# Optimization experiments

Measured on AMD Instinct MI355X. Metric: run time of the kernel, lower is better.

Reference implementation:

```python
import jax, jax.numpy as jnp
import numpy as np

H = 50  # hidden_dim
L = 4   # num_layers

def setup_inputs() -> dict:
    key = jax.random.key(0)
    ks = jax.random.split(key, 12)
    B, T, D = 2048, 512, 1
    s0 = 1.0 / np.sqrt(H)  # PyTorch GRU init scale
    x = jax.random.normal(ks[0], (B, T, D), dtype=jnp.float32)
    # layer 0 (input size 1)
    W_ih0 = jax.random.uniform(ks[1], (3 * H, D), minval=-s0, maxval=s0, dtype=jnp.float32)
    W_hh0 = jax.random.uniform(ks[2], (3 * H, H), minval=-s0, maxval=s0, dtype=jnp.float32)
    b_ih0 = jax.random.uniform(ks[3], (3 * H,), minval=-s0, maxval=s0, dtype=jnp.float32)
    b_hh0 = jax.random.uniform(ks[4], (3 * H,), minval=-s0, maxval=s0, dtype=jnp.float32)
    # layers 1..3 stacked (input size H)
    W_ih = jax.random.uniform(ks[5], (L - 1, 3 * H, H), minval=-s0, maxval=s0, dtype=jnp.float32)
    W_hh = jax.random.uniform(ks[6], (L - 1, 3 * H, H), minval=-s0, maxval=s0, dtype=jnp.float32)
    b_ih = jax.random.uniform(ks[7], (L - 1, 3 * H), minval=-s0, maxval=s0, dtype=jnp.float32)
    b_hh = jax.random.uniform(ks[8], (L - 1, 3 * H), minval=-s0, maxval=s0, dtype=jnp.float32)
    fc_w = jax.random.uniform(ks[9], (1, H), minval=-s0, maxval=s0, dtype=jnp.float32)
    fc_b = jax.random.uniform(ks[10], (1,), minval=-s0, maxval=s0, dtype=jnp.float32)
    return {"x": x, "W_ih0": W_ih0, "W_hh0": W_hh0, "b_ih0": b_ih0, "b_hh0": b_hh0,
            "W_ih": W_ih, "W_hh": W_hh, "b_ih": b_ih, "b_hh": b_hh,
            "fc_w": fc_w, "fc_b": fc_b}


def _gru_layer(x_seq, Wih, Whh, bih, bhh):
    # x_seq: [B, T, Din] -> outputs [B, T, H]. PyTorch GRU cell math.
    gx = jnp.einsum('btd,gd->btg', x_seq, Wih) + bih  # [B, T, 3H], precomputed input gates
    gx = jnp.transpose(gx, (1, 0, 2))  # [T, B, 3H]
    h0 = jnp.zeros((x_seq.shape[0], H), dtype=x_seq.dtype)

    def step(h, gxt):
        gh = h @ Whh.T + bhh  # [B, 3H]
        xr, xz, xn = jnp.split(gxt, 3, axis=-1)
        hr, hz, hn = jnp.split(gh, 3, axis=-1)
        r = jax.nn.sigmoid(xr + hr)
        z = jax.nn.sigmoid(xz + hz)
        n = jnp.tanh(xn + r * hn)
        h_new = (1.0 - z) * n + z * h
        return h_new, h_new

    _, hs = jax.lax.scan(step, h0, gx)  # hs: [T, B, H]
    return jnp.transpose(hs, (1, 0, 2))  # [B, T, H]


def reference(x, W_ih0, W_hh0, b_ih0, b_hh0, W_ih, W_hh, b_ih, b_hh, fc_w, fc_b):
    out = _gru_layer(x, W_ih0, W_hh0, b_ih0, b_hh0)
    for l in range(L - 1):  # eval mode: dropout inactive
        out = _gru_layer(out, W_ih[l], W_hh[l], b_ih[l], b_hh[l])
    last = out[:, -1, :]  # [B, H]
    logits = last @ fc_w.T + fc_b  # [B, 1]
    return jax.nn.sigmoid(logits)
```

## Files before the change

kernel.cpp:

```cpp
#include <hip/hip_runtime.h>
#include <hip/hip_fp16.h>

#define HDIM  50
#define G3    150
#define TSEQ  512
#define BATCH 2048
#define NB    8
#define NLAY  4
#define NT    12

typedef _Float16 f16x8 __attribute__((ext_vector_type(8)));
typedef float    f32x4 __attribute__((ext_vector_type(4)));

#define MFMA(a,b,c) __builtin_amdgcn_mfma_f32_16x16x32_f16((a),(b),(c),0,0,0)

static __device__ inline unsigned pk2(float a, float b) {
    return __builtin_bit_cast(unsigned, __builtin_amdgcn_cvt_pkrtz(a, b));
}
static __device__ inline float rcpf(float x) { return __builtin_amdgcn_rcpf(x); }

#if __has_builtin(__builtin_amdgcn_exp2f)
static __device__ inline float ex2(float x) { return __builtin_amdgcn_exp2f(x); }
#else
static __device__ inline float ex2(float x) {
    float r; asm volatile("v_exp_f32 %0, %1" : "=v"(r) : "v"(x)); return r;
}
#endif
static __device__ inline float dpp8(float x) {
    return __builtin_bit_cast(float, __builtin_amdgcn_mov_dpp(
        __builtin_bit_cast(int, x), 0x128, 0xf, 0xf, true));
}

#define SCL_RZ (-1.44269504f)
#define SCL_N  ( 2.88539008f)

__global__ __launch_bounds__(256, 1)
void gru_fused1w(const float* __restrict__ xin,
                 const float* __restrict__ Wih0, const float* __restrict__ Whh0,
                 const float* __restrict__ bih0, const float* __restrict__ bhh0,
                 const float* __restrict__ WihL, const float* __restrict__ WhhL,
                 const float* __restrict__ bihL, const float* __restrict__ bhhL,
                 const float* __restrict__ fcw,  const float* __restrict__ fcb,
                 float* __restrict__ out)
{
    const int tid  = threadIdx.x;
    const int lay  = tid >> 6;
    const int lane = tid & 63;
    const int lb   = lane & 15;
    const int lg   = lane >> 4;
    const int b0   = blockIdx.x * NB;
    const int lbc  = (lb < NB) ? lb : (NB - 1);
    const bool lo  = (lb < 8);

    __shared__ __align__(16) _Float16 h_lds[NLAY][2][16][72];
    __shared__ float x_row[NB][516];

    const float* Wih = (lay==0) ? Wih0 : WihL + (size_t)(lay-1)*G3*HDIM;
    const float* Whh = (lay==0) ? Whh0 : WhhL + (size_t)(lay-1)*G3*HDIM;
    const float* bih = (lay==0) ? bih0 : bihL + (lay-1)*G3;
    const float* bhh = (lay==0) ? bhh0 : bhhL + (lay-1)*G3;

    f16x8 a_hh[NT][2], a_ih[NT][2];
#pragma unroll
    for (int mt = 0; mt < NT; ++mt) {
        const int  ur = (mt & 3)*16 + lb;
        const bool rv = ur < HDIM;
        const int  gr = 50*(mt >> 2) + (rv ? ur : 0);
        const float scl = (mt < 8) ? SCL_RZ : SCL_N;
#pragma unroll
        for (int kt = 0; kt < 2; ++kt) {
            f16x8 fh, fi;
#pragma unroll
            for (int j = 0; j < 8; ++j) {
                const int k = 32*kt + 8*lg + j;
                float vh = 0.f, vi = 0.f;
                if (rv) {
                    if (k < HDIM)       vh = Whh[gr*HDIM + k];
                    else if (k == HDIM) vh = bhh[gr];
                    if (lay == 0) {
                        if (kt == 0 && k == 0)      vi = Wih[gr];
                        else if (kt == 0 && k == 1) vi = bih[gr];
                    } else {
                        if (k < HDIM)       vi = Wih[gr*HDIM + k];
                        else if (k == HDIM) vi = bih[gr];
                    }
                }
                fh[j] = (_Float16)(vh * scl); fi[j] = (_Float16)(vi * scl);
            }
            a_hh[mt][kt] = fh; a_ih[mt][kt] = fi;
        }
    }

    for (int k = tid; k < NB*TSEQ; k += 256)
        x_row[k >> 9][k & 511] = xin[(size_t)(b0 + (k >> 9))*TSEQ + (k & 511)];
    for (int k = tid; k < NLAY*2*16*72; k += 256)
        ((_Float16*)h_lds)[k] = (_Float16)(((k % 72) == HDIM) ? 1.f : 0.f);

    float hold[4][4];
#pragma unroll
    for (int m = 0; m < 4; ++m)
#pragma unroll
        for (int i = 0; i < 4; ++i) hold[m][i] = 0.f;
    __syncthreads();

    f16x8 bh0 = *(const f16x8*)&h_lds[lay][1][lb][8*lg];
    f16x8 bh1 = *(const f16x8*)&h_lds[lay][1][lb][32 + 8*lg];
    f16x8 bx0{}, bx1{};
    if (lay == 0) {
#pragma unroll
        for (int j = 0; j < 8; ++j) bx0[j] = (_Float16)0.f;
        if (lg == 0) { bx0[0] = (_Float16)x_row[lbc][0]; bx0[1] = (_Float16)1.f; }
    } else {
        bx0 = *(const f16x8*)&h_lds[lay-1][1][lb][8*lg];
        bx1 = *(const f16x8*)&h_lds[lay-1][1][lb][32 + 8*lg];
    }
    const f32x4 Z4 = {0.f, 0.f, 0.f, 0.f};

    for (int s = 0; s < TSEQ + NLAY - 1; ++s) {
        const int t = s - lay;
        if (t >= 0 && t < TSEQ) {
            f32x4 acc[NT], accx[4];
#pragma unroll
            for (int mt = 0; mt < NT; ++mt) acc[mt] = MFMA(a_hh[mt][0], bh0, Z4);
#pragma unroll
            for (int mt = 0; mt < NT; ++mt) acc[mt] = MFMA(a_hh[mt][1], bh1, acc[mt]);
#pragma unroll
            for (int mt = 0; mt < 8; ++mt)  acc[mt] = MFMA(a_ih[mt][0], bx0, acc[mt]);
#pragma unroll
            for (int m = 0; m < 4; ++m)     accx[m] = MFMA(a_ih[8+m][0], bx0, Z4);
            if (lay != 0) {
#pragma unroll
                for (int mt = 0; mt < 8; ++mt) acc[mt] = MFMA(a_ih[mt][1], bx1, acc[mt]);
#pragma unroll
                for (int m = 0; m < 4; ++m)    accx[m] = MFMA(a_ih[8+m][1], bx1, accx[m]);
            }

#pragma unroll
            for (int mt = 0; mt < 8; ++mt) {
#pragma unroll
                for (int ip = 0; ip < 2; ++ip) {
                    if (((mt & 3) == 3) && ip == 1) continue;
                    const float v0 = acc[mt][2*ip], v1 = acc[mt][2*ip+1];
                    const float w  = dpp8(v1);
                    const float sg = rcpf(1.f + ex2(lo ? v0 : w));
                    const float sb = dpp8(sg);
                    acc[mt][2*ip]   = lo ? sg : sb;
                    acc[mt][2*ip+1] = lo ? sb : sg;
                }
            }

            float hp[4][4];
#pragma unroll
            for (int m = 0; m < 4; ++m) {
#pragma unroll
                for (int ip = 0; ip < 2; ++ip) {
                    if (m == 3 && ip == 1) { hp[3][2] = 0.f; hp[3][3] = 0.f; continue; }
                    const int i0 = 2*ip, i1 = 2*ip + 1;
                    const float vp0 = accx[m][i0] + acc[m][i0] * acc[8+m][i0];
                    const float vp1 = accx[m][i1] + acc[m][i1] * acc[8+m][i1];
                    const float w   = dpp8(vp1);
                    const float n_  = 1.f - 2.f*rcpf(ex2(lo ? vp0 : w) + 1.f);
                    const float nb  = dpp8(n_);
                    const float n0  = lo ? n_ : nb;
                    const float n1  = lo ? nb : n_;
                    hp[m][i0] = fmaf(acc[4+m][i0], hold[m][i0] - n0, n0);
                    hp[m][i1] = fmaf(acc[4+m][i1], hold[m][i1] - n1, n1);
                    hold[m][i0] = hp[m][i0];
                    hold[m][i1] = hp[m][i1];
                }
            }

            {
                _Float16* hrow = &h_lds[lay][s & 1][lb][0];
#pragma unroll
                for (int m = 0; m < 3; ++m) {
                    uint2 q; q.x = pk2(hp[m][0], hp[m][1]);
                             q.y = pk2(hp[m][2], hp[m][3]);
                    *(uint2*)&hrow[16*m + 4*lg] = q;
                }
                if (lg == 0)
                    *(unsigned*)&hrow[48] = pk2(hp[3][0], hp[3][1]);
            }
        }
        __syncthreads();

        const int pb = s & 1;
        bh0 = *(const f16x8*)&h_lds[lay][pb][lb][8*lg];
        bh1 = *(const f16x8*)&h_lds[lay][pb][lb][32 + 8*lg];
        if (lay == 0) {
            const int tt = (s+1 < TSEQ) ? s+1 : TSEQ-1;
            if (lg == 0) bx0[0] = (_Float16)x_row[lbc][tt];
        } else {
            bx0 = *(const f16x8*)&h_lds[lay-1][pb][lb][8*lg];
            bx1 = *(const f16x8*)&h_lds[lay-1][pb][lb][32 + 8*lg];
        }
    }

    if (tid < NB) {
        float sacc = fcb[0];
#pragma unroll
        for (int j = 0; j < HDIM; ++j)
            sacc = fmaf((float)h_lds[NLAY-1][0][tid][j], fcw[j], sacc);
        out[b0 + tid] = rcpf(1.f + __expf(-sacc));
    }
}

extern "C" void kernel_launch(void* const* d_in, const int* in_sizes, int n_in,
                              void* d_out, int out_size, void* d_ws, size_t ws_size,
                              hipStream_t stream) {
    const float* x     = (const float*)d_in[0];
    const float* W_ih0 = (const float*)d_in[1];
    const float* W_hh0 = (const float*)d_in[2];
    const float* b_ih0 = (const float*)d_in[3];
    const float* b_hh0 = (const float*)d_in[4];
    const float* W_ih  = (const float*)d_in[5];
    const float* W_hh  = (const float*)d_in[6];
    const float* b_ih  = (const float*)d_in[7];
    const float* b_hh  = (const float*)d_in[8];
    const float* fc_w  = (const float*)d_in[9];
    const float* fc_b  = (const float*)d_in[10];
    float* out = (float*)d_out;

    dim3 grid(BATCH / NB), block(256);
    gru_fused1w<<<grid, block, 0, stream>>>(
        x, W_ih0, W_hh0, b_ih0, b_hh0,
        W_ih, W_hh, b_ih, b_hh, fc_w, fc_b, out);
}
```

Before: 596.1 us.

## Process two timesteps per barrier with 4-slot hidden-state ring buffer

```diff
diff --git a/kernel.cpp b/kernel.cpp
--- a/kernel.cpp
+++ b/kernel.cpp
@@ -52,7 +52,7 @@
     const int lbc  = (lb < NB) ? lb : (NB - 1);
     const bool lo  = (lb < 8);
 
-    __shared__ __align__(16) _Float16 h_lds[NLAY][2][16][72];
+    __shared__ __align__(16) _Float16 hsl[NLAY][4][16][72];
     __shared__ float x_row[NB][516];
 
     const float* Wih = (lay==0) ? Wih0 : WihL + (size_t)(lay-1)*G3*HDIM;
@@ -93,8 +93,8 @@
 
     for (int k = tid; k < NB*TSEQ; k += 256)
         x_row[k >> 9][k & 511] = xin[(size_t)(b0 + (k >> 9))*TSEQ + (k & 511)];
-    for (int k = tid; k < NLAY*2*16*72; k += 256)
-        ((_Float16*)h_lds)[k] = (_Float16)(((k % 72) == HDIM) ? 1.f : 0.f);
+    for (int k = tid; k < NLAY*4*16*72; k += 256)
+        ((_Float16*)hsl)[k] = (_Float16)(((k % 72) == HDIM) ? 1.f : 0.f);
 
     float hold[4][4];
 #pragma unroll
@@ -103,104 +103,106 @@
         for (int i = 0; i < 4; ++i) hold[m][i] = 0.f;
     __syncthreads();
 
-    f16x8 bh0 = *(const f16x8*)&h_lds[lay][1][lb][8*lg];
-    f16x8 bh1 = *(const f16x8*)&h_lds[lay][1][lb][32 + 8*lg];
-    f16x8 bx0{}, bx1{};
-    if (lay == 0) {
-#pragma unroll
-        for (int j = 0; j < 8; ++j) bx0[j] = (_Float16)0.f;
-        if (lg == 0) { bx0[0] = (_Float16)x_row[lbc][0]; bx0[1] = (_Float16)1.f; }
-    } else {
-        bx0 = *(const f16x8*)&h_lds[lay-1][1][lb][8*lg];
-        bx1 = *(const f16x8*)&h_lds[lay-1][1][lb][32 + 8*lg];
-    }
+    f16x8 bh0 = *(const f16x8*)&hsl[lay][3][lb][8*lg];
+    f16x8 bh1 = *(const f16x8*)&hsl[lay][3][lb][32 + 8*lg];
     const f32x4 Z4 = {0.f, 0.f, 0.f, 0.f};
 
-    for (int s = 0; s < TSEQ + NLAY - 1; ++s) {
-        const int t = s - lay;
-        if (t >= 0 && t < TSEQ) {
-            f32x4 acc[NT], accx[4];
-#pragma unroll
-            for (int mt = 0; mt < NT; ++mt) acc[mt] = MFMA(a_hh[mt][0], bh0, Z4);
-#pragma unroll
-            for (int mt = 0; mt < NT; ++mt) acc[mt] = MFMA(a_hh[mt][1], bh1, acc[mt]);
-#pragma unroll
-            for (int mt = 0; mt < 8; ++mt)  acc[mt] = MFMA(a_ih[mt][0], bx0, acc[mt]);
-#pragma unroll
-            for (int m = 0; m < 4; ++m)     accx[m] = MFMA(a_ih[8+m][0], bx0, Z4);
-            if (lay != 0) {
-#pragma unroll
-                for (int mt = 0; mt < 8; ++mt) acc[mt] = MFMA(a_ih[mt][1], bx1, acc[mt]);
-#pragma unroll
-                for (int m = 0; m < 4; ++m)    accx[m] = MFMA(a_ih[8+m][1], bx1, accx[m]);
-            }
-
-#pragma unroll
-            for (int mt = 0; mt < 8; ++mt) {
-#pragma unroll
-                for (int ip = 0; ip < 2; ++ip) {
-                    if (((mt & 3) == 3) && ip == 1) continue;
-                    const float v0 = acc[mt][2*ip], v1 = acc[mt][2*ip+1];
-                    const float w  = dpp8(v1);
-                    const float sg = rcpf(1.f + ex2(lo ? v0 : w));
-                    const float sb = dpp8(sg);
-                    acc[mt][2*ip]   = lo ? sg : sb;
-                    acc[mt][2*ip+1] = lo ? sb : sg;
+    auto STEP = [&](int t, f16x8 bxk0, f16x8 bxk1) {
+        f32x4 acc[NT], accx[4];
+#pragma unroll
+        for (int mt = 0; mt < NT; ++mt) acc[mt] = MFMA(a_hh[mt][0], bh0, Z4);
+#pragma unroll
+        for (int mt = 0; mt < NT; ++mt) acc[mt] = MFMA(a_hh[mt][1], bh1, acc[mt]);
+#pragma unroll
+        for (int mt = 0; mt < 8; ++mt)  acc[mt] = MFMA(a_ih[mt][0], bxk0, acc[mt]);
+#pragma unroll
+        for (int m = 0; m < 4; ++m)     accx[m] = MFMA(a_ih[8+m][0], bxk0, Z4);
+        if (lay != 0) {
+#pragma unroll
+            for (int mt = 0; mt < 8; ++mt) acc[mt] = MFMA(a_ih[mt][1], bxk1, acc[mt]);
+#pragma unroll
+            for (int m = 0; m < 4; ++m)    accx[m] = MFMA(a_ih[8+m][1], bxk1, accx[m]);
+        }
+
+#pragma unroll
+        for (int mt = 0; mt < 8; ++mt) {
+#pragma unroll
+            for (int ip = 0; ip < 2; ++ip) {
+                if (((mt & 3) == 3) && ip == 1) continue;
+                const float v0 = acc[mt][2*ip], v1 = acc[mt][2*ip+1];
+                const float w  = dpp8(v1);
+                const float sg = rcpf(1.f + ex2(lo ? v0 : w));
+                const float sb = dpp8(sg);
+                acc[mt][2*ip]   = lo ? sg : sb;
+                acc[mt][2*ip+1] = lo ? sb : sg;
+            }
+        }
+
+        float hp[4][4];
+#pragma unroll
+        for (int m = 0; m < 4; ++m) {
+#pragma unroll
+            for (int ip = 0; ip < 2; ++ip) {
+                if (m == 3 && ip == 1) { hp[3][2] = 0.f; hp[3][3] = 0.f; continue; }
+                const int i0 = 2*ip, i1 = 2*ip + 1;
+                const float vp0 = accx[m][i0] + acc[m][i0] * acc[8+m][i0];
+                const float vp1 = accx[m][i1] + acc[m][i1] * acc[8+m][i1];
+                const float w   = dpp8(vp1);
+                const float n_  = 1.f - 2.f*rcpf(ex2(lo ? vp0 : w) + 1.f);
+                const float nb  = dpp8(n_);
+                const float n0  = lo ? n_ : nb;
+                const float n1  = lo ? nb : n_;
+                hp[m][i0] = fmaf(acc[4+m][i0], hold[m][i0] - n0, n0);
+                hp[m][i1] = fmaf(acc[4+m][i1], hold[m][i1] - n1, n1);
+                hold[m][i0] = hp[m][i0];
+                hold[m][i1] = hp[m][i1];
+            }
+        }
+
+        {
+            _Float16* hrow = &hsl[lay][t & 3][lb][0];
+#pragma unroll
+            for (int m = 0; m < 3; ++m) {
+                uint2 q; q.x = pk2(hp[m][0], hp[m][1]);
+                         q.y = pk2(hp[m][2], hp[m][3]);
+                *(uint2*)&hrow[16*m + 4*lg] = q;
+            }
+            if (lg == 0)
+                *(unsigned*)&hrow[48] = pk2(hp[3][0], hp[3][1]);
+        }
+        bh0 = *(const f16x8*)&hsl[lay][t & 3][lb][8*lg];
+        bh1 = *(const f16x8*)&hsl[lay][t & 3][lb][32 + 8*lg];
+    };
+
+    for (int s = 0; s < TSEQ/2 + NLAY - 1; ++s) {
+        if (s >= lay && s < lay + TSEQ/2) {
+            const int t0 = 2*(s - lay);
+            f16x8 bxa0{}, bxa1{}, bxb0{}, bxb1{};
+            if (lay == 0) {
+#pragma unroll
+                for (int j = 0; j < 8; ++j) { bxa0[j] = (_Float16)0.f; bxb0[j] = (_Float16)0.f; }
+                if (lg == 0) {
+                    bxa0[0] = (_Float16)x_row[lbc][t0];     bxa0[1] = (_Float16)1.f;
+                    bxb0[0] = (_Float16)x_row[lbc][t0 + 1]; bxb0[1] = (_Float16)1.f;
                 }
-            }
-
-            float hp[4][4];
-#pragma unroll
-            for (int m = 0; m < 4; ++m) {
-#pragma unroll
-                for (int ip = 0; ip < 2; ++ip) {
-                    if (m == 3 && ip == 1) { hp[3][2] = 0.f; hp[3][3] = 0.f; continue; }
-                    const int i0 = 2*ip, i1 = 2*ip + 1;
-                    const float vp0 = accx[m][i0] + acc[m][i0] * acc[8+m][i0];
-                    const float vp1 = accx[m][i1] + acc[m][i1] * acc[8+m][i1];
-                    const float w   = dpp8(vp1);
-                    const float n_  = 1.f - 2.f*rcpf(ex2(lo ? vp0 : w) + 1.f);
-                    const float nb  = dpp8(n_);
-                    const float n0  = lo ? n_ : nb;
-                    const float n1  = lo ? nb : n_;
-                    hp[m][i0] = fmaf(acc[4+m][i0], hold[m][i0] - n0, n0);
-                    hp[m][i1] = fmaf(acc[4+m][i1], hold[m][i1] - n1, n1);
-                    hold[m][i0] = hp[m][i0];
-                    hold[m][i1] = hp[m][i1];
-                }
-            }
-
-            {
-                _Float16* hrow = &h_lds[lay][s & 1][lb][0];
-#pragma unroll
-                for (int m = 0; m < 3; ++m) {
-                    uint2 q; q.x = pk2(hp[m][0], hp[m][1]);
-                             q.y = pk2(hp[m][2], hp[m][3]);
-                    *(uint2*)&hrow[16*m + 4*lg] = q;
-                }
-                if (lg == 0)
-                    *(unsigned*)&hrow[48] = pk2(hp[3][0], hp[3][1]);
-            }
+            } else {
+                const int sa = t0 & 3, sb = (t0 + 1) & 3;
+                bxa0 = *(const f16x8*)&hsl[lay-1][sa][lb][8*lg];
+                bxa1 = *(const f16x8*)&hsl[lay-1][sa][lb][32 + 8*lg];
+                bxb0 = *(const f16x8*)&hsl[lay-1][sb][lb][8*lg];
+                bxb1 = *(const f16x8*)&hsl[lay-1][sb][lb][32 + 8*lg];
+            }
+            STEP(t0,     bxa0, bxa1);
+            STEP(t0 + 1, bxb0, bxb1);
         }
         __syncthreads();
-
-        const int pb = s & 1;
-        bh0 = *(const f16x8*)&h_lds[lay][pb][lb][8*lg];
-        bh1 = *(const f16x8*)&h_lds[lay][pb][lb][32 + 8*lg];
-        if (lay == 0) {
-            const int tt = (s+1 < TSEQ) ? s+1 : TSEQ-1;
-            if (lg == 0) bx0[0] = (_Float16)x_row[lbc][tt];
-        } else {
-            bx0 = *(const f16x8*)&h_lds[lay-1][pb][lb][8*lg];
-            bx1 = *(const f16x8*)&h_lds[lay-1][pb][lb][32 + 8*lg];
-        }
     }
 
     if (tid < NB) {
         float sacc = fcb[0];
 #pragma unroll
         for (int j = 0; j < HDIM; ++j)
-            sacc = fmaf((float)h_lds[NLAY-1][0][tid][j], fcw[j], sacc);
+            sacc = fmaf((float)hsl[NLAY-1][3][tid][j], fcw[j], sacc);
         out[b0 + tid] = rcpf(1.f + __expf(-sacc));
     }
 }
```

Result: no change. 589.0 us (-1.2%).
